# Kernel optimization log

Measured on AMD Instinct MI355X. Metric: run time of the kernel, lower is better.

## Reference

```python
import jax, jax.numpy as jnp
import numpy as np

NTOKEN = 32000
NINP = 512
NHIDLAST = 1024
N_EXPERTS = 10
N = 1024


def setup_inputs() -> dict:
    key = jax.random.key(0)
    ks = jax.random.split(key, 4)
    return {
        "output": jax.random.normal(ks[0], (N, NHIDLAST), dtype=jnp.float32),
        "W_latent": jax.random.normal(ks[1], (N_EXPERTS * NINP, NHIDLAST), dtype=jnp.float32) * 0.02,
        "b_latent": jnp.zeros((N_EXPERTS * NINP,), dtype=jnp.float32),
        "W_decoder": jax.random.normal(ks[2], (NTOKEN, NINP), dtype=jnp.float32) * 0.02,
        "b_decoder": jnp.zeros((NTOKEN,), dtype=jnp.float32),
        "W_reduce": jax.random.normal(ks[3], (N_EXPERTS, NHIDLAST), dtype=jnp.float32) * 0.02,
        "b_reduce": jnp.zeros((N_EXPERTS,), dtype=jnp.float32),
        "dropoutl": 0,
    }


def reference(output, W_latent, b_latent, W_decoder, b_decoder, W_reduce, b_reduce, dropoutl):
    n = output.shape[0]
    # latent projection + tanh; lockdrop with rate 0 is identity
    latent = jnp.tanh(output @ W_latent.T + b_latent)            # [N, E*ninp]
    logit = latent.reshape(n * N_EXPERTS, NINP) @ W_decoder.T + b_decoder  # [N*E, V]
    # stick-breaking Beta parameters
    a = jax.nn.softplus(output @ W_reduce.T + b_reduce) + 1e-8   # [N, E]
    b = jnp.sum(a, axis=1)                                       # [N]
    c = jnp.cumsum(a, axis=1)                                    # [N, E]
    d = jnp.abs(b[:, None] - c)                                  # remaining mass
    d = jnp.maximum(d, 1e-8)  # last column is exactly 0; avoid Beta(a,0) NaN
    sample = jax.random.beta(jax.random.key(42), a, d)           # reparameterized Beta
    # rem @ diag(ones, offset=1) shifts columns right by one; rem[:,0]=1
    rem = 1.0 - sample
    rem_shift = jnp.concatenate([jnp.ones((n, 1), dtype=rem.dtype), rem[:, :-1]], axis=1)
    remprod = jnp.cumprod(rem_shift, axis=1)
    pis = remprod * sample                                       # [N, E] mixture weights
    prob = jax.nn.softmax(logit.reshape(n, N_EXPERTS, NTOKEN), axis=-1)
    out = jnp.einsum('net,ne->nt', prob, pis)                    # [N, V]
    return out
```

## Files before the change

kernel.cpp:

```cpp
#include <hip/hip_runtime.h>
#include <cstdint>
#include <cstddef>

#pragma clang fp contract(off)

#define NTOK  32000
#define NINP  512
#define NHID  1024
#define NEXP  10
#define NROW  1024
#define NLAT  (NEXP*NINP)
#define MROWS (NROW*NEXP)

typedef __attribute__((ext_vector_type(4))) float f32x4;
typedef __attribute__((ext_vector_type(8))) short bf16x8;
typedef __attribute__((ext_vector_type(8))) unsigned short us16x8;

#define GLD16(g, l) __builtin_amdgcn_global_load_lds(                       \
    (const __attribute__((address_space(1))) void*)(g),                     \
    (__attribute__((address_space(3))) void*)(l), 16, 0, 0)

__device__ __forceinline__ unsigned short f2b(float x) {
    uint32_t u = __float_as_uint(x);
    uint32_t r = (u + 0x7fffu + ((u >> 16) & 1u)) >> 16;
    return (unsigned short)r;
}
__device__ __forceinline__ float b2f(unsigned short b) {
    return __uint_as_float(((uint32_t)b) << 16);
}

__device__ __forceinline__ uint32_t rotl32(uint32_t v, int r) {
    return (v << r) | (v >> (32 - r));
}

__device__ __forceinline__ void threefry(uint32_t k0, uint32_t k1,
                                         uint32_t x0, uint32_t x1,
                                         uint32_t& o0, uint32_t& o1) {
    uint32_t k2 = k0 ^ k1 ^ 0x1BD11BDAu;
    x0 += k0; x1 += k1;
#define TF_R(r) { x0 += x1; x1 = rotl32(x1, r); x1 ^= x0; }
    TF_R(13) TF_R(15) TF_R(26) TF_R(6)
    x0 += k1; x1 += k2 + 1u;
    TF_R(17) TF_R(29) TF_R(16) TF_R(24)
    x0 += k2; x1 += k0 + 2u;
    TF_R(13) TF_R(15) TF_R(26) TF_R(6)
    x0 += k0; x1 += k1 + 3u;
    TF_R(17) TF_R(29) TF_R(16) TF_R(24)
    x0 += k1; x1 += k2 + 4u;
    TF_R(13) TF_R(15) TF_R(26) TF_R(6)
    x0 += k2; x1 += k0 + 5u;
#undef TF_R
    o0 = x0; o1 = x1;
}

struct RKey { uint32_t a, b; };

__device__ __forceinline__ RKey kfold(RKey k, uint32_t i) {
    RKey r; threefry(k.a, k.b, 0u, i, r.a, r.b); return r;
}
__device__ __forceinline__ uint32_t kbits(RKey k) {
    uint32_t o0, o1; threefry(k.a, k.b, 0u, 0u, o0, o1); return o0 ^ o1;
}
__device__ __forceinline__ float u01(RKey k) {
    uint32_t b = (kbits(k) >> 9) | 0x3f800000u;
    return __uint_as_float(b) - 1.0f;
}
__device__ __forceinline__ float erfinv_xla(float x) {
    float xx = x * x;
    float w = -log1pf(-xx);
    float p;
    if (w < 5.0f) {
        float ww = w - 2.5f;
        p = 2.81022636e-08f;
        p = p * ww; p = p + 3.43273939e-07f;
        p = p * ww; p = p + -3.5233877e-06f;
        p = p * ww; p = p + -4.39150654e-06f;
        p = p * ww; p = p + 0.00021858087f;
        p = p * ww; p = p + -0.00125372503f;
        p = p * ww; p = p + -0.00417768164f;
        p = p * ww; p = p + 0.246640727f;
        p = p * ww; p = p + 1.50140941f;
    } else {
        float ww = sqrtf(w) - 3.0f;
        p = -0.000200214257f;
        p = p * ww; p = p + 0.000100950558f;
        p = p * ww; p = p + 0.00134934322f;
        p = p * ww; p = p + -0.00367342844f;
        p = p * ww; p = p + 0.00573950773f;
        p = p * ww; p = p + -0.0076224613f;
        p = p * ww; p = p + 0.00943887047f;
        p = p * ww; p = p + 1.00167406f;
        p = p * ww; p = p + 2.83297682f;
    }
    return p * x;
}
__device__ __forceinline__ float norm1(RKey k) {
    const float lo = -0.99999994f;
    float f = u01(k);
    float u = f * 2.0f;
    u = u + lo;
    u = fmaxf(lo, u);
    return 1.41421356f * erfinv_xla(u);
}

__device__ float gamma_log(RKey key, float alpha) {
    const float one_third = 0.33333334f;
    bool boost = (alpha >= 1.0f);
    float alpha_orig = alpha;
    if (!boost) alpha = alpha + 1.0f;
    float d = alpha - one_third;
    float c = one_third / sqrtf(d);

    RKey sub = kfold(key, 1u);
    key      = kfold(key, 0u);
    float log_boost = 0.0f;
    if (!boost) {
        float uB = u01(sub);
        log_boost = log1pf(-uB) * (1.0f / alpha_orig);
    }

    float X = 0.f, V = 1.f, U = 2.f;
    int guard = 0;
    do {
        RKey xk = kfold(key, 1u);
        RKey Uk = kfold(key, 2u);
        key     = kfold(key, 0u);
        float x = 0.f, v = -1.f;
        RKey kin = xk;
        int g2 = 0;
        do {
            RKey sk = kfold(kin, 1u);
            kin     = kfold(kin, 0u);
            x = norm1(sk);
            float cx = x * c;
            v = 1.0f + cx;
        } while (v <= 0.0f && ++g2 < 256);
        X = x * x;
        V = (v * v) * v;
        U = u01(Uk);
        float sq = 1.0f - 0.0331f * (X * X);
        if (U < sq) break;
        float bound = (X * 0.5f) + ((d - d * V) + d * logf(V));
        if (logf(U) < bound) break;
    } while (++guard < 256);

    float ls = logf(d) + logf(V);
    ls = ls + log_boost;
    return ls;
}

__global__ void k_a(const float* __restrict__ out_in,
                    const float* __restrict__ Wred,
                    const float* __restrict__ bred,
                    float* __restrict__ a_arr, float* __restrict__ dpar) {
    int n = blockIdx.x;
    int lane = threadIdx.x;
    __shared__ float zred[NEXP];
    const float* orow = out_in + (size_t)n * NHID;
    for (int e = 0; e < NEXP; ++e) {
        const float* wrow = Wred + (size_t)e * NHID;
        float s = 0.f;
        for (int k = lane; k < NHID; k += 64) s += orow[k] * wrow[k];
        for (int off = 32; off; off >>= 1) s += __shfl_xor(s, off);
        if (lane == 0) zred[e] = s + bred[e];
    }
    __syncthreads();
    if (lane == 0) {
        float a[NEXP];
        float b = 0.f;
        for (int e = 0; e < NEXP; ++e) {
            float z = zred[e];
            a[e] = fmaxf(z, 0.f) + log1pf(expf(-fabsf(z))) + 1e-8f;
        }
        for (int e = 0; e < NEXP; ++e) b += a[e];
        float cs = 0.f;
        for (int e = 0; e < NEXP; ++e) {
            cs += a[e];
            float dd = fmaxf(fabsf(b - cs), 1e-8f);
            a_arr[n * NEXP + e] = a[e];
            dpar [n * NEXP + e] = dd;
        }
    }
}

__global__ void k_sample(const float* __restrict__ a_arr,
                         const float* __restrict__ dpar,
                         float* __restrict__ sample) {
    int i = blockIdx.x * 256 + threadIdx.x;
    if (i >= MROWS) return;
    RKey root{0u, 42u};
    RKey ka = kfold(root, 0u);
    RKey kb = kfold(root, 1u);
    float lga = gamma_log(kfold(ka, (uint32_t)i), a_arr[i]);
    float lgb = gamma_log(kfold(kb, (uint32_t)i), dpar[i]);
    float lm = fmaxf(lga, lgb);
    float ea = expf(lga - lm), eb = expf(lgb - lm);
    sample[i] = ea / (ea + eb);
}

__global__ void k_pis(const float* __restrict__ sample, float* __restrict__ pis) {
    int n = blockIdx.x * blockDim.x + threadIdx.x;
    if (n >= NROW) return;
    float rp = 1.0f;
    for (int e = 0; e < NEXP; ++e) {
        float s = sample[n * NEXP + e];
        pis[n * NEXP + e] = rp * s;
        rp = rp * (1.0f - s);
    }
}

__global__ void k_w(const float* __restrict__ pis, const float* __restrict__ Z,
                    float* __restrict__ w, int r0, int cnt) {
    int i = blockIdx.x * 256 + threadIdx.x;
    if (i >= cnt) return;
    int r = r0 + i;
    w[r] = pis[r] / Z[r];
}

__global__ void k_cvt(const float* __restrict__ src, unsigned short* __restrict__ dst, int n) {
    int i = (blockIdx.x * 256 + threadIdx.x) * 8;
    if (i >= n) return;
    float4 v0 = *(const float4*)(src + i);
    float4 v1 = *(const float4*)(src + i + 4);
    us16x8 o;
    o[0] = f2b(v0.x); o[1] = f2b(v0.y); o[2] = f2b(v0.z); o[3] = f2b(v0.w);
    o[4] = f2b(v1.x); o[5] = f2b(v1.y); o[6] = f2b(v1.z); o[7] = f2b(v1.w);
    *(us16x8*)(dst + i) = o;
}

__global__ __launch_bounds__(256)
void k_latm(const unsigned short* __restrict__ A,
            const unsigned short* __restrict__ B,
            const float* __restrict__ bias,
            unsigned short* __restrict__ dst) {
    __shared__ unsigned short Als[2][128 * 64];
    __shared__ unsigned short Bls[2][128 * 64];
    const int tid  = threadIdx.x;
    const int lane = tid & 63, wid = tid >> 6;
    const int wm = wid >> 1, wn = wid & 1;
    const uint32_t l = blockIdx.x;
    const int row0 = (int)(l & 7u) * 128;
    const int col0 = (int)(l >> 3) * 128;
    const int lrow8 = lane >> 3, lslot = lane & 7;

    const unsigned short* pA[4];
    const unsigned short* pB[4];
#pragma unroll
    for (int i = 0; i < 4; ++i) {
        int rA = wid * 32 + i * 8 + lrow8;
        pA[i] = A + (size_t)(row0 + rA) * NHID + ((lslot ^ (rA & 7)) << 3);
        int rB = wid * 32 + i * 8 + lrow8;
        pB[i] = B + (size_t)(col0 + rB) * NHID + ((lslot ^ (rB & 7)) << 3);
    }
    int offA[2][4], offB[2][4];
#pragma unroll
    for (int kh = 0; kh < 2; ++kh)
#pragma unroll
        for (int f = 0; f < 4; ++f) {
            int rA = wm * 64 + f * 16 + (lane & 15);
            offA[kh][f] = rA * 128 + ((((lane >> 4) * 16) + kh * 64) ^ ((rA & 7) << 4));
            int rB = wn * 64 + f * 16 + (lane & 15);
            offB[kh][f] = rB * 128 + ((((lane >> 4) * 16) + kh * 64) ^ ((rB & 7) << 4));
        }

    f32x4 acc[4][4];
#pragma unroll
    for (int mf = 0; mf < 4; ++mf)
#pragma unroll
        for (int nf = 0; nf < 4; ++nf) acc[mf][nf] = (f32x4)0.f;

#pragma unroll
    for (int i = 0; i < 4; ++i) {
        GLD16(pA[i], (char*)&Als[0][0] + (wid * 32 + i * 8) * 128); pA[i] += 64;
        GLD16(pB[i], (char*)&Bls[0][0] + (wid * 32 + i * 8) * 128); pB[i] += 64;
    }
    __syncthreads();

#pragma unroll
    for (int t = 0; t < 16; ++t) {
        const int cur = t & 1, nxt = cur ^ 1;
        if (t < 15) {
#pragma unroll
            for (int i = 0; i < 4; ++i) {
                GLD16(pA[i], (char*)&Als[nxt][0] + (wid * 32 + i * 8) * 128); pA[i] += 64;
                GLD16(pB[i], (char*)&Bls[nxt][0] + (wid * 32 + i * 8) * 128); pB[i] += 64;
            }
        }
        const char* Ab = (const char*)&Als[cur][0];
        const char* Bb = (const char*)&Bls[cur][0];
#pragma unroll
        for (int kh = 0; kh < 2; ++kh) {
            bf16x8 af[4], bfr[4];
#pragma unroll
            for (int f = 0; f < 4; ++f) {
                af[f]  = *(const bf16x8*)(Ab + offA[kh][f]);
                bfr[f] = *(const bf16x8*)(Bb + offB[kh][f]);
            }
#pragma unroll
            for (int mf = 0; mf < 4; ++mf)
#pragma unroll
                for (int nf = 0; nf < 4; ++nf)
                    acc[mf][nf] = __builtin_amdgcn_mfma_f32_16x16x32_bf16(
                        af[mf], bfr[nf], acc[mf][nf], 0, 0, 0);
        }
        __syncthreads();
    }

    const int q = lane >> 4, cl = lane & 15;
#pragma unroll
    for (int mf = 0; mf < 4; ++mf) {
#pragma unroll
        for (int nf = 0; nf < 4; ++nf) {
            int col = col0 + wn * 64 + nf * 16 + cl;
            float bc = bias[col];
#pragma unroll
            for (int j = 0; j < 4; ++j) {
                int r = row0 + wm * 64 + mf * 16 + q * 4 + j;
                dst[(size_t)r * NLAT + col] = f2b(tanhf(acc[mf][nf][j] + bc));
            }
        }
    }
}

template<int MODE>
__global__ __launch_bounds__(256)
void k_dec(const unsigned short* __restrict__ A,
           const unsigned short* __restrict__ B,
           const float* __restrict__ bias,
           const float* __restrict__ wmix,
           float* __restrict__ dst,
           unsigned short* __restrict__ Pst,
           int rb0, int nRB) {
    __shared__ unsigned short Als[2][160 * 64];
    __shared__ unsigned short Bls[2][128 * 64];
    const int tid  = threadIdx.x;
    const int lane = tid & 63, wid = tid >> 6;
    const int wm = wid >> 1, wn = wid & 1;
    const uint32_t l = blockIdx.x;
    int by_l, bx;
    if (nRB >= 8) {
        const int per = nRB >> 3;
        const uint32_t jb = l >> 3;
        by_l = (int)(l & 7u) * per + (int)(jb % (uint32_t)per);
        bx   = (int)(jb / (uint32_t)per);
    } else {
        by_l = (int)(l % (uint32_t)nRB);
        bx   = (int)(l / (uint32_t)nRB);
    }
    const int by   = rb0 + by_l;
    const int row0 = by * 160;
    const int rl0  = by_l * 160;
    const int col0 = bx * 128;
    const int lrow8 = lane >> 3, lslot = lane & 7;

    const unsigned short* pA[5];
    const unsigned short* pB[4];
#pragma unroll
    for (int i = 0; i < 5; ++i) {
        int rA = wid * 40 + i * 8 + lrow8;
        pA[i] = A + (size_t)(row0 + rA) * 512 + ((lslot ^ (rA & 7)) << 3);
    }
#pragma unroll
    for (int i = 0; i < 4; ++i) {
        int rB = wid * 32 + i * 8 + lrow8;
        pB[i] = B + (size_t)(col0 + rB) * 512 + ((lslot ^ (rB & 7)) << 3);
    }
    int offA[2][5], offB[2][4];
#pragma unroll
    for (int kh = 0; kh < 2; ++kh) {
#pragma unroll
        for (int mf = 0; mf < 5; ++mf) {
            int r = wm * 80 + mf * 16 + (lane & 15);
            offA[kh][mf] = r * 128 + ((((lane >> 4) * 16) + kh * 64) ^ ((r & 7) << 4));
        }
#pragma unroll
        for (int nf = 0; nf < 4; ++nf) {
            int r = wn * 64 + nf * 16 + (lane & 15);
            offB[kh][nf] = r * 128 + ((((lane >> 4) * 16) + kh * 64) ^ ((r & 7) << 4));
        }
    }

    f32x4 acc[5][4];
#pragma unroll
    for (int mf = 0; mf < 5; ++mf)
#pragma unroll
        for (int nf = 0; nf < 4; ++nf) acc[mf][nf] = (f32x4)0.f;

#pragma unroll
    for (int i = 0; i < 5; ++i) {
        GLD16(pA[i], (char*)&Als[0][0] + (wid * 40 + i * 8) * 128); pA[i] += 64;
    }
#pragma unroll
    for (int i = 0; i < 4; ++i) {
        GLD16(pB[i], (char*)&Bls[0][0] + (wid * 32 + i * 8) * 128); pB[i] += 64;
    }
    __syncthreads();

#pragma unroll
    for (int t = 0; t < 8; ++t) {
        const int cur = t & 1, nxt = cur ^ 1;
        if (t < 7) {
#pragma unroll
            for (int i = 0; i < 5; ++i) {
                GLD16(pA[i], (char*)&Als[nxt][0] + (wid * 40 + i * 8) * 128); pA[i] += 64;
            }
#pragma unroll
            for (int i = 0; i < 4; ++i) {
                GLD16(pB[i], (char*)&Bls[nxt][0] + (wid * 32 + i * 8) * 128); pB[i] += 64;
            }
        }
        const char* Ab = (const char*)&Als[cur][0];
        const char* Bb = (const char*)&Bls[cur][0];
#pragma unroll
        for (int kh = 0; kh < 2; ++kh) {
            bf16x8 af[5], bfr[4];
#pragma unroll
            for (int mf = 0; mf < 5; ++mf)
                af[mf] = *(const bf16x8*)(Ab + offA[kh][mf]);
#pragma unroll
            for (int nf = 0; nf < 4; ++nf)
                bfr[nf] = *(const bf16x8*)(Bb + offB[kh][nf]);
#pragma unroll
            for (int mf = 0; mf < 5; ++mf)
#pragma unroll
                for (int nf = 0; nf < 4; ++nf)
                    acc[mf][nf] = __builtin_amdgcn_mfma_f32_16x16x32_bf16(
                        af[mf], bfr[nf], acc[mf][nf], 0, 0, 0);
        }
        __syncthreads();
    }

    const int q = lane >> 4, cl = lane & 15;
    float bv[4];
#pragma unroll
    for (int nf = 0; nf < 4; ++nf) bv[nf] = bias[col0 + wn * 64 + nf * 16 + cl];

    if (MODE == 1 || MODE == 3) {
#pragma unroll
        for (int mf = 0; mf < 5; ++mf) {
#pragma unroll
            for (int jj = 0; jj < 4; ++jj) {
                const int rr = wm * 80 + mf * 16 + q * 4 + jj;
                float p0 = expf(acc[mf][0][jj] + bv[0]);
                float p1 = expf(acc[mf][1][jj] + bv[1]);
                float p2 = expf(acc[mf][2][jj] + bv[2]);
                float p3 = expf(acc[mf][3][jj] + bv[3]);
                float s = ((p0 + p1) + (p2 + p3));
                s += __shfl_xor(s, 1); s += __shfl_xor(s, 2);
                s += __shfl_xor(s, 4); s += __shfl_xor(s, 8);
                if (cl == 0) atomicAdd(&dst[row0 + rr], s);
                if (MODE == 3) {
                    unsigned short* prow =
                        Pst + (size_t)(rl0 + rr) * NTOK + col0 + wn * 64 + cl;
                    prow[0]  = f2b(p0);
                    prow[16] = f2b(p1);
                    prow[32] = f2b(p2);
                    prow[48] = f2b(p3);
                }
            }
        }
    } else {
        float wv[5][4];
#pragma unroll
        for (int mf = 0; mf < 5; ++mf)
#pragma unroll
            for (int jj = 0; jj < 4; ++jj)
                wv[mf][jj] = wmix[row0 + wm * 80 + mf * 16 + q * 4 + jj];
#pragma unroll
        for (int mf = 0; mf < 5; ++mf)
#pragma unroll
            for (int nf = 0; nf < 4; ++nf)
#pragma unroll
                for (int jj = 0; jj < 4; ++jj)
                    acc[mf][nf][jj] = wv[mf][jj] * expf(acc[mf][nf][jj] + bv[nf]);

        const int tok0 = by * 16 + wm * 8;
#pragma unroll
        for (int t = 0; t < 8; ++t) {
#pragma unroll
            for (int nf = 0; nf < 4; ++nf) {
                float s = 0.f;
#pragma unroll
                for (int i = 0; i < 10; ++i) {
                    const int rl = 10 * t + i;
                    const int mf = rl >> 4, qr = (rl >> 2) & 3, jj = rl & 3;
                    s += (q == qr) ? acc[mf][nf][jj] : 0.f;
                }
                s += __shfl_xor(s, 16);
                s += __shfl_xor(s, 32);
                if (q == 0)
                    dst[(size_t)(tok0 + t) * NTOK + col0 + wn * 64 + nf * 16 + cl] = s;
            }
        }
    }
}

__global__ __launch_bounds__(256)
void k_fin(const unsigned short* __restrict__ P,
           const float* __restrict__ pis,
           const float* __restrict__ Z,
           float* __restrict__ out, int n0) {
    uint32_t gid = blockIdx.x * 256u + threadIdx.x;
    uint32_t nl = gid / 4000u;
    uint32_t c8 = (gid - nl * 4000u) * 8u;
    uint32_t n  = n0 + nl;
    float w[NEXP];
#pragma unroll
    for (int e = 0; e < NEXP; ++e)
        w[e] = pis[n * NEXP + e] / Z[n * NEXP + e];
    float s[8] = {0.f,0.f,0.f,0.f,0.f,0.f,0.f,0.f};
    const unsigned short* Pr = P + (size_t)nl * NEXP * NTOK + c8;
#pragma unroll
    for (int e = 0; e < NEXP; ++e) {
        us16x8 v = *(const us16x8*)(Pr + (size_t)e * NTOK);
#pragma unroll
        for (int jj = 0; jj < 8; ++jj)
            s[jj] = s[jj] + w[e] * b2f(v[jj]);
    }
    float* orow = out + (size_t)n * NTOK + c8;
    float4 o0 = {s[0], s[1], s[2], s[3]};
    float4 o1 = {s[4], s[5], s[6], s[7]};
    *(float4*)(orow)     = o0;
    *(float4*)(orow + 4) = o1;
}

extern "C" void kernel_launch(void* const* d_in, const int* in_sizes, int n_in,
                              void* d_out, int out_size, void* d_ws, size_t ws_size,
                              hipStream_t stream) {
    const float* output    = (const float*)d_in[0];
    const float* W_latent  = (const float*)d_in[1];
    const float* b_latent  = (const float*)d_in[2];
    const float* W_decoder = (const float*)d_in[3];
    const float* b_decoder = (const float*)d_in[4];
    const float* W_reduce  = (const float*)d_in[5];
    const float* b_reduce  = (const float*)d_in[6];
    float* out = (float*)d_out;

    char* wsb = (char*)d_ws;
    unsigned short* latb  = (unsigned short*)wsb;
    unsigned short* wdecb = (unsigned short*)(wsb + 10485760);
    float* a_arr  = (float*)(wsb + 10485760 + 32768000);
    float* dpar   = a_arr  + MROWS;
    float* sample = dpar   + MROWS;
    float* pis    = sample + MROWS;
    float* Z      = pis    + MROWS;
    float* wmix   = Z      + MROWS;
    unsigned short* Pbuf = (unsigned short*)(wmix + MROWS);
    const size_t BASE = 10485760ull + 32768000ull + 6ull * MROWS * 4ull;
    const size_t avail = (ws_size > BASE) ? (ws_size - BASE) : 0;
    int CR = 0;
    {
        const int cands[5] = {2560, 1280, 640, 320, 160};
        for (int c = 0; c < 5; ++c)
            if ((size_t)cands[c] * NTOK * 2ull <= avail) { CR = cands[c]; break; }
    }

    unsigned short* outb  = (unsigned short*)d_out;
    unsigned short* wlatb = (unsigned short*)((char*)d_out + 2097152);

    k_a<<<NROW, 64, 0, stream>>>(output, W_reduce, b_reduce, a_arr, dpar);
    k_sample<<<MROWS / 256, 256, 0, stream>>>(a_arr, dpar, sample);
    k_pis<<<(NROW + 255) / 256, 256, 0, stream>>>(sample, pis);

    k_cvt<<<(NTOK * NINP) / 2048, 256, 0, stream>>>(W_decoder, wdecb, NTOK * NINP);
    k_cvt<<<(NROW * NHID) / 2048, 256, 0, stream>>>(output, outb, NROW * NHID);
    k_cvt<<<(NLAT * NHID) / 2048, 256, 0, stream>>>(W_latent, wlatb, NLAT * NHID);

    k_latm<<<320, 256, 0, stream>>>(outb, wlatb, b_latent, latb);

    (void)hipMemsetAsync(Z, 0, MROWS * sizeof(float), stream);

    if (CR > 0) {
        const int nRB = CR / 160;
        for (int r0 = 0; r0 < MROWS; r0 += CR) {
            k_dec<3><<<nRB * 250, 256, 0, stream>>>(latb, wdecb, b_decoder,
                                                    nullptr, Z, Pbuf, r0 / 160, nRB);
            k_fin<<<(CR / 10) * 4000 / 256, 256, 0, stream>>>(Pbuf, pis, Z,
                                                              out, r0 / 10);
        }
    } else {
        k_dec<1><<<16000, 256, 0, stream>>>(latb, wdecb, b_decoder,
                                            nullptr, Z, nullptr, 0, 64);
        k_w<<<MROWS / 256, 256, 0, stream>>>(pis, Z, wmix, 0, MROWS);
        k_dec<2><<<16000, 256, 0, stream>>>(latb, wdecb, b_decoder,
                                            wmix, out, nullptr, 0, 64);
    }
    (void)in_sizes; (void)n_in; (void)out_size;
}
```

Before: 860.1 us.

## Double-buffer decoder chunks and fuse previous chunk's combine into GEMM launch

The probability staging buffer is split into two halves. Each decoder GEMM launch gets extra blocks that run the weighted expert combine for the previous chunk, so the memory-bound combine overlaps with the compute-bound GEMM instead of running as its own serialized kernel. Stores of the staged bf16 probabilities and the final output, and loads in the combine, now use nontemporal hints to reduce cache pollution. This halves the usable chunk size for a given workspace. It also relies on the previous chunk's softmax denominators Z being complete before the next launch, which in-order stream execution guarantees.

```diff
diff --git a/kernel.cpp b/kernel.cpp
--- a/kernel.cpp
+++ b/kernel.cpp
@@ -228,6 +228,46 @@
     *(us16x8*)(dst + i) = o;
 }
 
+__device__ __forceinline__ void combine_span(const unsigned short* __restrict__ P,
+                                             const float* __restrict__ pis,
+                                             const float* __restrict__ Z,
+                                             float* __restrict__ out,
+                                             int n0, int items, int idx0, int stride) {
+    for (int idx = idx0; idx < items; idx += stride) {
+        int nl = idx / 4000;
+        int c8 = (idx - nl * 4000) * 8;
+        int n  = n0 + nl;
+        float w[NEXP];
+#pragma unroll
+        for (int e = 0; e < NEXP; ++e)
+            w[e] = pis[n * NEXP + e] / Z[n * NEXP + e];
+        float s[8] = {0.f,0.f,0.f,0.f,0.f,0.f,0.f,0.f};
+        const unsigned short* Pr = P + (size_t)nl * NEXP * NTOK + c8;
+#pragma unroll
+        for (int e = 0; e < NEXP; ++e) {
+            us16x8 v = __builtin_nontemporal_load((const us16x8*)(Pr + (size_t)e * NTOK));
+#pragma unroll
+            for (int jj = 0; jj < 8; ++jj)
+                s[jj] = s[jj] + w[e] * b2f(v[jj]);
+        }
+        float* orow = out + (size_t)n * NTOK + c8;
+        f32x4 o0 = {s[0], s[1], s[2], s[3]};
+        f32x4 o1 = {s[4], s[5], s[6], s[7]};
+        __builtin_nontemporal_store(o0, (f32x4*)(orow));
+        __builtin_nontemporal_store(o1, (f32x4*)(orow + 4));
+    }
+}
+
+__global__ __launch_bounds__(256)
+void k_fin(const unsigned short* __restrict__ P,
+           const float* __restrict__ pis,
+           const float* __restrict__ Z,
+           float* __restrict__ out, int n0, int items) {
+    combine_span(P, pis, Z, out, n0, items,
+                 (int)(blockIdx.x * 256u + threadIdx.x),
+                 (int)(gridDim.x * 256u));
+}
+
 __global__ __launch_bounds__(256)
 void k_latm(const unsigned short* __restrict__ A,
             const unsigned short* __restrict__ B,
@@ -330,7 +370,19 @@
            const float* __restrict__ wmix,
            float* __restrict__ dst,
            unsigned short* __restrict__ Pst,
-           int rb0, int nRB) {
+           int rb0, int nRB, int nGemm,
+           const float* __restrict__ pis,
+           const float* __restrict__ Zarr,
+           float* __restrict__ outp,
+           const unsigned short* __restrict__ Pprev,
+           int n0prev, int itemsPrev) {
+    if (MODE == 3 && (int)blockIdx.x >= nGemm) {
+        const int cb = (int)blockIdx.x - nGemm;
+        combine_span(Pprev, pis, Zarr, outp, n0prev, itemsPrev,
+                     cb * 256 + (int)threadIdx.x,
+                     ((int)gridDim.x - nGemm) * 256);
+        return;
+    }
     __shared__ unsigned short Als[2][160 * 64];
     __shared__ unsigned short Bls[2][128 * 64];
     const int tid  = threadIdx.x;
@@ -452,10 +504,10 @@
                 if (MODE == 3) {
                     unsigned short* prow =
                         Pst + (size_t)(rl0 + rr) * NTOK + col0 + wn * 64 + cl;
-                    prow[0]  = f2b(p0);
-                    prow[16] = f2b(p1);
-                    prow[32] = f2b(p2);
-                    prow[48] = f2b(p3);
+                    __builtin_nontemporal_store(f2b(p0), prow);
+                    __builtin_nontemporal_store(f2b(p1), prow + 16);
+                    __builtin_nontemporal_store(f2b(p2), prow + 32);
+                    __builtin_nontemporal_store(f2b(p3), prow + 48);
                 }
             }
         }
@@ -493,35 +545,6 @@
             }
         }
     }
-}
-
-__global__ __launch_bounds__(256)
-void k_fin(const unsigned short* __restrict__ P,
-           const float* __restrict__ pis,
-           const float* __restrict__ Z,
-           float* __restrict__ out, int n0) {
-    uint32_t gid = blockIdx.x * 256u + threadIdx.x;
-    uint32_t nl = gid / 4000u;
-    uint32_t c8 = (gid - nl * 4000u) * 8u;
-    uint32_t n  = n0 + nl;
-    float w[NEXP];
-#pragma unroll
-    for (int e = 0; e < NEXP; ++e)
-        w[e] = pis[n * NEXP + e] / Z[n * NEXP + e];
-    float s[8] = {0.f,0.f,0.f,0.f,0.f,0.f,0.f,0.f};
-    const unsigned short* Pr = P + (size_t)nl * NEXP * NTOK + c8;
-#pragma unroll
-    for (int e = 0; e < NEXP; ++e) {
-        us16x8 v = *(const us16x8*)(Pr + (size_t)e * NTOK);
-#pragma unroll
-        for (int jj = 0; jj < 8; ++jj)
-            s[jj] = s[jj] + w[e] * b2f(v[jj]);
-    }
-    float* orow = out + (size_t)n * NTOK + c8;
-    float4 o0 = {s[0], s[1], s[2], s[3]};
-    float4 o1 = {s[4], s[5], s[6], s[7]};
-    *(float4*)(orow)     = o0;
-    *(float4*)(orow + 4) = o1;
 }
 
 extern "C" void kernel_launch(void* const* d_in, const int* in_sizes, int n_in,
@@ -548,11 +571,17 @@
     unsigned short* Pbuf = (unsigned short*)(wmix + MROWS);
     const size_t BASE = 10485760ull + 32768000ull + 6ull * MROWS * 4ull;
     const size_t avail = (ws_size > BASE) ? (ws_size - BASE) : 0;
-    int CR = 0;
+
+    int CRd = 0, CRs = 0;
     {
-        const int cands[5] = {2560, 1280, 640, 320, 160};
-        for (int c = 0; c < 5; ++c)
-            if ((size_t)cands[c] * NTOK * 2ull <= avail) { CR = cands[c]; break; }
+        const int cands[4] = {2560, 1280, 640, 320};
+        for (int c = 0; c < 4; ++c)
+            if (2ull * (size_t)cands[c] * NTOK * 2ull <= avail) { CRd = cands[c]; break; }
+        if (CRd == 0) {
+            const int cs[5] = {2560, 1280, 640, 320, 160};
+            for (int c = 0; c < 5; ++c)
+                if ((size_t)cs[c] * NTOK * 2ull <= avail) { CRs = cs[c]; break; }
+        }
     }
 
     unsigned short* outb  = (unsigned short*)d_out;
@@ -570,20 +599,37 @@
 
     (void)hipMemsetAsync(Z, 0, MROWS * sizeof(float), stream);
 
-    if (CR > 0) {
-        const int nRB = CR / 160;
-        for (int r0 = 0; r0 < MROWS; r0 += CR) {
-            k_dec<3><<<nRB * 250, 256, 0, stream>>>(latb, wdecb, b_decoder,
-                                                    nullptr, Z, Pbuf, r0 / 160, nRB);
-            k_fin<<<(CR / 10) * 4000 / 256, 256, 0, stream>>>(Pbuf, pis, Z,
-                                                              out, r0 / 10);
+    if (CRd > 0) {
+        const int nRB = CRd / 160, nGemm = nRB * 250, nch = MROWS / CRd;
+        const int items = (CRd / 10) * 4000;
+        for (int ci = 0; ci < nch; ++ci) {
+            unsigned short* Pcur  = Pbuf + (size_t)(ci & 1) * CRd * NTOK;
+            unsigned short* Pprev = Pbuf + (size_t)((ci & 1) ^ 1) * CRd * NTOK;
+            const int extra = (ci > 0) ? 1000 : 0;
+            k_dec<3><<<nGemm + extra, 256, 0, stream>>>(
+                latb, wdecb, b_decoder, nullptr, Z, Pcur, ci * nRB, nRB, nGemm,
+                pis, Z, out, Pprev, (ci - 1) * (CRd / 10), items);
+        }
+        unsigned short* Plast = Pbuf + (size_t)((nch - 1) & 1) * CRd * NTOK;
+        k_fin<<<items / 256, 256, 0, stream>>>(Plast, pis, Z, out,
+                                               (nch - 1) * (CRd / 10), items);
+    } else if (CRs > 0) {
+        const int nRB = CRs / 160;
+        const int items = (CRs / 10) * 4000;
+        for (int r0 = 0; r0 < MROWS; r0 += CRs) {
+            k_dec<3><<<nRB * 250, 256, 0, stream>>>(
+                latb, wdecb, b_decoder, nullptr, Z, Pbuf, r0 / 160, nRB, 1 << 30,
+                pis, Z, out, nullptr, 0, 0);
+            k_fin<<<items / 256, 256, 0, stream>>>(Pbuf, pis, Z, out, r0 / 10, items);
         }
     } else {
-        k_dec<1><<<16000, 256, 0, stream>>>(latb, wdecb, b_decoder,
-                                            nullptr, Z, nullptr, 0, 64);
+        k_dec<1><<<16000, 256, 0, stream>>>(latb, wdecb, b_decoder, nullptr, Z,
+                                            nullptr, 0, 64, 1 << 30,
+                                            pis, Z, out, nullptr, 0, 0);
         k_w<<<MROWS / 256, 256, 0, stream>>>(pis, Z, wmix, 0, MROWS);
-        k_dec<2><<<16000, 256, 0, stream>>>(latb, wdecb, b_decoder,
-                                            wmix, out, nullptr, 0, 64);
+        k_dec<2><<<16000, 256, 0, stream>>>(latb, wdecb, b_decoder, wmix, out,
+                                            nullptr, 0, 64, 1 << 30,
+                                            pis, Z, out, nullptr, 0, 0);
     }
     (void)in_sizes; (void)n_in; (void)out_size;
 }
```

New measurement: 831.5 us. -3.3%, faster.
